# Kernel optimization log

Hardware: AMD Instinct MI355X
Metric: run time of the kernel (lower is better)

## Reference

```python
import jax, jax.numpy as jnp
import numpy as np

Ts = 1.0  # simulation time step from netParams['simulation']


def _alpha_filter(x, tau):
    # Causal SRM-alpha PSP filter along time (leading axis):
    #   y[t] = Ts * sum_{k>=0} (k*Ts/tau) * exp(1 - k*Ts/tau) * x[t-k]
    # Implemented as an exact 2-state linear recurrence (IIR form of the alpha kernel).
    d = jnp.float32(np.exp(-Ts / tau))
    c = jnp.float32(np.e * Ts / tau * Ts)  # kernel scale * Ts integration factor

    def step(carry, xt):
        P, Q = carry           # P[t] = sum x[j] d^{t-j}; Q[t] = sum x[j] (t-j) d^{t-j}
        Q = d * (Q + P)
        P = d * P + xt
        return (P, Q), c * Q

    z = jnp.zeros_like(x[0])
    _, y = jax.lax.scan(step, (z, z), x)
    return y


def _make_spike(theta, tauRho, scaleRho):
    # SLAYER spike function: Heaviside forward, surrogate-gradient backward
    pdf_scale = scaleRho / (tauRho * theta)
    pdf_tc = tauRho * theta

    @jax.custom_vjp
    def spike(u):
        return (u >= theta).astype(u.dtype)

    def fwd(u):
        return spike(u), u

    def bwd(u, g):
        return (g * pdf_scale * jnp.exp(-jnp.abs(u - theta) / pdf_tc),)

    spike.defvjp(fwd, bwd)
    return spike


def _lif_spike(u_in, theta, tauRef, scaleRef, tauRho, scaleRho):
    # Sequential leaky integrate-and-fire with alpha refractory kernel:
    #   u[t] = u_in[t] - scaleRef*theta * sum_{j<t} s[j] * (dt/tauRef)*exp(1-dt/tauRef), dt=(t-j)*Ts
    # Refractory alpha kernel realized by the same 2-state recurrence, fed by emitted spikes.
    d = jnp.float32(np.exp(-Ts / tauRef))
    ref_gain = jnp.float32(scaleRef * theta * np.e * Ts / tauRef)
    spike = _make_spike(theta, tauRho, scaleRho)

    def step(carry, ut):
        P, Q = carry
        Q = d * (Q + P)            # refractory kernel value (zero at lag 0)
        s = spike(ut - ref_gain * Q)
        P = d * P + s              # inject this step's spikes
        return (P, Q), s

    z = jnp.zeros_like(u_in[0])
    _, s = jax.lax.scan(step, (z, z), u_in)
    return s


def _conv2d_t(x, w, pad):
    # x: [T, N, C, H, W] -> same spatial conv applied at every timestep (slayer conv = Conv3d with kT=1)
    T, N, C, H, W = x.shape
    y = jax.lax.conv_general_dilated(
        x.reshape(T * N, C, H, W), w,
        window_strides=(1, 1), padding=[(pad, pad), (pad, pad)],
        dimension_numbers=('NCHW', 'OIHW', 'NCHW'))
    return y.reshape(T, N, -1, H, W)


def _forward(spikeInput, conv1_w, conv2_w):
    # spikeInput: [N, C, H, W, T] -> scan over leading time axis
    x = jnp.transpose(spikeInput, (4, 0, 1, 2, 3))
    psp1 = _alpha_filter(x, tau=1.0)                                        # slayer1.psp (tauSr=1)
    s1 = _lif_spike(_conv2d_t(psp1, conv1_w, 2),
                    theta=30.0, tauRef=1.0, scaleRef=1.0, tauRho=1.0, scaleRho=10.0)
    psp2 = _alpha_filter(s1, tau=2.0)                                       # slayer2.psp (tauSr=2)
    s2 = _lif_spike(_conv2d_t(psp2, conv2_w, 1),
                    theta=50.0, tauRef=2.0, scaleRef=1.0, tauRho=1.0, scaleRho=10.0)
    return jnp.transpose(s2, (1, 2, 3, 4, 0))  # back to [N, C, H, W, T]


def setup_inputs() -> dict:
    key = jax.random.key(0)
    k1, k2, k3 = jax.random.split(key, 3)
    spikeInput = (jax.random.uniform(k1, (2, 8, 128, 128, 64)) < 0.1).astype(jnp.float32)
    # slayer conv uses weightScale-amplified weights, bias-free; scale so thresholds are reachable
    conv1_w = jax.random.normal(k2, (8, 8, 5, 5), jnp.float32) * 2.0
    conv2_w = jax.random.normal(k3, (8, 8, 3, 3), jnp.float32) * 2.0
    return {"spikeInput": spikeInput, "conv1_w": conv1_w, "conv2_w": conv2_w}


def reference(spikeInput, conv1_w, conv2_w):
    return _forward(spikeInput, conv1_w, conv2_w)
```

## Files before the change

kernel.cpp:

```cpp
#include <hip/hip_runtime.h>

#define TN 64
#define NB 2
#define CH 8
#define HH 128
#define WW 128
#define HW (HH*WW)
#define CHW (CH*HW)
#define NCHW (NB*CHW)


__global__ __launch_bounds__(256) void k_tr(const float* __restrict__ x,
                                            unsigned char* __restrict__ xT) {
    __shared__ unsigned char lds[256 * 68];
    const int tid = threadIdx.x;
    const size_t e0 = (size_t)blockIdx.x * 256;
    const float4* xb = reinterpret_cast<const float4*>(x + (e0 + tid) * TN);
    unsigned int* lds32 = reinterpret_cast<unsigned int*>(lds);
    #pragma unroll
    for (int k = 0; k < 16; ++k) {
        float4 v = xb[k];
        unsigned int p = ((unsigned)v.x) | (((unsigned)v.y) << 8) |
                         (((unsigned)v.z) << 16) | (((unsigned)v.w) << 24);
        lds32[tid * 17 + k] = p;
    }
    __syncthreads();
    const int lane = tid & 63, w = tid >> 6;
    #pragma unroll
    for (int k = 0; k < 16; ++k) {
        int t = w * 16 + k;
        unsigned int b0 = lds[(4 * lane + 0) * 68 + t];
        unsigned int b1 = lds[(4 * lane + 1) * 68 + t];
        unsigned int b2 = lds[(4 * lane + 2) * 68 + t];
        unsigned int b3 = lds[(4 * lane + 3) * 68 + t];
        unsigned int p = b0 | (b1 << 8) | (b2 << 16) | (b3 << 24);
        *reinterpret_cast<unsigned int*>(xT + (size_t)t * NCHW + e0 + 4 * lane) = p;
    }
}

__global__ __launch_bounds__(256, 4) void k_conv1(const unsigned char* __restrict__ in,
                                                  const float* __restrict__ w1,
                                                  float* __restrict__ outp) {
    __shared__ __align__(16) float tile[2][12][136];
    const int img = blockIdx.y;
    const int h0 = blockIdx.x * 8;
    const int tid = threadIdx.x;
    const int yi = tid >> 5;
    const int x0 = (tid & 31) * 4;
    const unsigned char* base = in + (size_t)img * CHW;

    int goff[7];
    #pragma unroll
    for (int k = 0; k < 7; ++k) {
        int idx = tid + (k << 8);
        int r = idx / 136;
        int c = idx - r * 136;
        int gh = h0 + r - 2, gw = c - 2;
        bool ok = (idx < 1632) && (gh >= 0) && (gh < HH) && (gw >= 0) && (gw < WW);
        goff[k] = ok ? (gh * WW + gw) : -1;
    }

    float va[7];
    #pragma unroll
    for (int k = 0; k < 7; ++k) {
        int g = goff[k];
        int gc = g < 0 ? 0 : g;
        float t0 = (float)base[gc];
        va[k] = g < 0 ? 0.f : t0;
    }

    float acc[CH][4];
    #pragma unroll
    for (int co = 0; co < CH; ++co)
        #pragma unroll
        for (int xo = 0; xo < 4; ++xo) acc[co][xo] = 0.f;

    for (int ci = 0; ci < CH; ++ci) {
        float* dst = &tile[ci & 1][0][0];
        #pragma unroll
        for (int k = 0; k < 7; ++k) {
            int idx = tid + (k << 8);
            if (k < 6 || idx < 1632) dst[idx] = va[k];
        }
        if (ci < 7) {
            const unsigned char* nb = base + (size_t)(ci + 1) * HW;
            #pragma unroll
            for (int k = 0; k < 7; ++k) {
                int g = goff[k];
                int gc = g < 0 ? 0 : g;
                float t0 = (float)nb[gc];
                va[k] = g < 0 ? 0.f : t0;
            }
        }
        __syncthreads();

        const float* chp = &tile[ci & 1][0][0];
        #pragma unroll
        for (int ky = 0; ky < 5; ++ky) {
            const float4* rp =
                reinterpret_cast<const float4*>(chp + (yi + ky) * 136 + x0);
            float4 A = rp[0], B = rp[1];
            float f[8] = {A.x, A.y, A.z, A.w, B.x, B.y, B.z, B.w};
            #pragma unroll
            for (int co = 0; co < CH; ++co) {
                const float* wp = w1 + (co * CH + ci) * 25 + ky * 5;
                #pragma unroll
                for (int kx = 0; kx < 5; ++kx) {
                    float wv = wp[kx];
                    #pragma unroll
                    for (int xo = 0; xo < 4; ++xo)
                        acc[co][xo] = fmaf(wv, f[kx + xo], acc[co][xo]);
                }
            }
        }
    }

    float* ob = outp + (size_t)img * CHW + (h0 + yi) * WW + x0;
    #pragma unroll
    for (int co = 0; co < CH; ++co)
        *reinterpret_cast<float4*>(ob + co * HW) =
            make_float4(acc[co][0], acc[co][1], acc[co][2], acc[co][3]);
}

__global__ __launch_bounds__(256) void k_alif1(const float* __restrict__ v1,
                                               unsigned char* __restrict__ s1) {
    int e2 = blockIdx.x * blockDim.x + threadIdx.x;
    if (e2 >= NCHW / 2) return;
    const float d1 = 0.36787944117144233f;
    const float c1 = 2.7182818284590452f;
    const float dr = 0.36787944117144233f;
    const float rg = 81.54845485377136f;
    const float th = 30.f;
    float P0 = 0.f, Q0 = 0.f, Pr0 = 0.f, Qr0 = 0.f;
    float P1 = 0.f, Q1 = 0.f, Pr1 = 0.f, Qr1 = 0.f;
    const float2* ve = reinterpret_cast<const float2*>(v1);
    #pragma unroll 8
    for (int t = 0; t < TN; ++t) {
        float2 v = ve[(size_t)t * (NCHW / 2) + e2];
        Q0 = d1 * (Q0 + P0); P0 = d1 * P0 + v.x;
        Qr0 = dr * (Qr0 + Pr0);
        float s0 = (c1 * Q0 - rg * Qr0 >= th) ? 1.0f : 0.0f;
        Pr0 = dr * Pr0 + s0;
        Q1 = d1 * (Q1 + P1); P1 = d1 * P1 + v.y;
        Qr1 = dr * (Qr1 + Pr1);
        float s1v = (c1 * Q1 - rg * Qr1 >= th) ? 1.0f : 0.0f;
        Pr1 = dr * Pr1 + s1v;
        uchar2 o; o.x = (unsigned char)s0; o.y = (unsigned char)s1v;
        *reinterpret_cast<uchar2*>(s1 + (size_t)t * NCHW + 2 * e2) = o;
    }
}

__global__ __launch_bounds__(256, 4) void k_conv2(const unsigned char* __restrict__ in,
                                                  const float* __restrict__ w2,
                                                  float* __restrict__ outp) {
    __shared__ __align__(16) float tile[2][10][136];
    const int img = blockIdx.y;
    const int h0 = blockIdx.x * 8;
    const int tid = threadIdx.x;
    const int yi = tid >> 5;
    const int x0 = (tid & 31) * 4;
    const unsigned char* base = in + (size_t)img * CHW;

    int goff[6];
    #pragma unroll
    for (int k = 0; k < 6; ++k) {
        int idx = tid + (k << 8);
        int r = idx / 136;
        int c = idx - r * 136;
        int gh = h0 + r - 1, gw = c - 1;
        bool ok = (idx < 1360) && (gh >= 0) && (gh < HH) && (gw >= 0) && (gw < WW);
        goff[k] = ok ? (gh * WW + gw) : -1;
    }

    float va[6];
    #pragma unroll
    for (int k = 0; k < 6; ++k) {
        int g = goff[k];
        int gc = g < 0 ? 0 : g;
        float t0 = (float)base[gc];
        va[k] = g < 0 ? 0.f : t0;
    }

    float acc[CH][4];
    #pragma unroll
    for (int co = 0; co < CH; ++co)
        #pragma unroll
        for (int xo = 0; xo < 4; ++xo) acc[co][xo] = 0.f;

    for (int ci = 0; ci < CH; ++ci) {
        float* dst = &tile[ci & 1][0][0];
        #pragma unroll
        for (int k = 0; k < 6; ++k) {
            int idx = tid + (k << 8);
            if (k < 5 || idx < 1360) dst[idx] = va[k];
        }
        if (ci < 7) {
            const unsigned char* nb = base + (size_t)(ci + 1) * HW;
            #pragma unroll
            for (int k = 0; k < 6; ++k) {
                int g = goff[k];
                int gc = g < 0 ? 0 : g;
                float t0 = (float)nb[gc];
                va[k] = g < 0 ? 0.f : t0;
            }
        }
        __syncthreads();

        const float* chp = &tile[ci & 1][0][0];
        #pragma unroll
        for (int ky = 0; ky < 3; ++ky) {
            const float4* rp =
                reinterpret_cast<const float4*>(chp + (yi + ky) * 136 + x0);
            float4 A = rp[0], B = rp[1];
            float f[8] = {A.x, A.y, A.z, A.w, B.x, B.y, B.z, B.w};
            #pragma unroll
            for (int co = 0; co < CH; ++co) {
                const float* wp = w2 + (co * CH + ci) * 9 + ky * 3;
                #pragma unroll
                for (int kx = 0; kx < 3; ++kx) {
                    float wv = wp[kx];
                    #pragma unroll
                    for (int xo = 0; xo < 4; ++xo)
                        acc[co][xo] = fmaf(wv, f[kx + xo], acc[co][xo]);
                }
            }
        }
    }

    float* ob = outp + (size_t)img * CHW + (h0 + yi) * WW + x0;
    #pragma unroll
    for (int co = 0; co < CH; ++co)
        *reinterpret_cast<float4*>(ob + co * HW) =
            make_float4(acc[co][0], acc[co][1], acc[co][2], acc[co][3]);
}

__global__ __launch_bounds__(256) void k_alif2(const float* __restrict__ v2,
                                               float* __restrict__ outp) {
    int e = blockIdx.x * blockDim.x + threadIdx.x;
    if (e >= NCHW) return;
    const float d2 = 0.60653065971263342f;
    const float c2 = 1.35914091422952262f;
    const float dr = 0.60653065971263342f;
    const float rg = 67.95704571147613f;
    const float th = 50.f;
    float P = 0.f, Q = 0.f, Pr = 0.f, Qr = 0.f;
    float sv[TN];
    #pragma unroll
    for (int t = 0; t < TN; ++t) {
        Q = d2 * (Q + P);
        P = d2 * P + v2[(size_t)t * NCHW + e];
        Qr = dr * (Qr + Pr);
        float s = (c2 * Q - rg * Qr >= th) ? 1.0f : 0.0f;
        Pr = dr * Pr + s;
        sv[t] = s;
    }
    float4* o = reinterpret_cast<float4*>(outp + (size_t)e * TN);
    #pragma unroll
    for (int i = 0; i < TN / 4; ++i)
        o[i] = make_float4(sv[4 * i], sv[4 * i + 1], sv[4 * i + 2], sv[4 * i + 3]);
}

extern "C" void kernel_launch(void* const* d_in, const int* in_sizes, int n_in,
                              void* d_out, int out_size, void* d_ws, size_t ws_size,
                              hipStream_t stream) {
    const float* x  = (const float*)d_in[0];
    const float* w1 = (const float*)d_in[1];
    const float* w2 = (const float*)d_in[2];
    float* out = (float*)d_out;

    float* vbuf = (float*)d_ws;
    unsigned char* xT = (unsigned char*)d_ws + (size_t)TN * NCHW * 4;
    unsigned char* s1 = xT + (size_t)TN * NCHW;

    dim3 blk(256);
    dim3 grd_pt(NCHW / 256);
    dim3 grd_pt2(NCHW / 512);
    dim3 grd_cv(16, TN * NB);

    k_tr<<<grd_pt, blk, 0, stream>>>(x, xT);
    k_conv1<<<grd_cv, blk, 0, stream>>>(xT, w1, vbuf);
    k_alif1<<<grd_pt2, blk, 0, stream>>>(vbuf, s1);
    k_conv2<<<grd_cv, blk, 0, stream>>>(s1, w2, vbuf);
    k_alif2<<<grd_pt, blk, 0, stream>>>(vbuf, out);
}
```

Before: 180.8 us.

## Stage all input channels as bytes in shared memory with a single barrier

Both convolution kernels now load all eight input channels of the halo tile into shared memory as uint8 values up front, followed by one barrier. This replaces the double-buffered float tile that synchronised once per channel. Each thread reads two 32-bit words per row and unpacks the bytes to floats in registers, which cuts shared-memory footprint and removes seven of the eight barriers. The cost is byte-extraction and int-to-float conversion work in the inner loop, and all global loads are issued before any compute starts instead of overlapping with it.

```diff
diff --git a/kernel.cpp b/kernel.cpp
--- a/kernel.cpp
+++ b/kernel.cpp
@@ -41,7 +41,7 @@
 __global__ __launch_bounds__(256, 4) void k_conv1(const unsigned char* __restrict__ in,
                                                   const float* __restrict__ w1,
                                                   float* __restrict__ outp) {
-    __shared__ __align__(16) float tile[2][12][136];
+    __shared__ __align__(16) unsigned char lds8[CH * 12 * 136];
     const int img = blockIdx.y;
     const int h0 = blockIdx.x * 8;
     const int tid = threadIdx.x;
@@ -60,47 +60,39 @@
         goff[k] = ok ? (gh * WW + gw) : -1;
     }
 
-    float va[7];
-    #pragma unroll
-    for (int k = 0; k < 7; ++k) {
-        int g = goff[k];
-        int gc = g < 0 ? 0 : g;
-        float t0 = (float)base[gc];
-        va[k] = g < 0 ? 0.f : t0;
-    }
-
-    float acc[CH][4];
-    #pragma unroll
-    for (int co = 0; co < CH; ++co)
-        #pragma unroll
-        for (int xo = 0; xo < 4; ++xo) acc[co][xo] = 0.f;
-
-    for (int ci = 0; ci < CH; ++ci) {
-        float* dst = &tile[ci & 1][0][0];
+    #pragma unroll
+    for (int ci = 0; ci < CH; ++ci) {
+        const unsigned char* cb = base + ci * HW;
         #pragma unroll
         for (int k = 0; k < 7; ++k) {
             int idx = tid + (k << 8);
-            if (k < 6 || idx < 1632) dst[idx] = va[k];
-        }
-        if (ci < 7) {
-            const unsigned char* nb = base + (size_t)(ci + 1) * HW;
-            #pragma unroll
-            for (int k = 0; k < 7; ++k) {
+            if (k < 6 || idx < 1632) {
                 int g = goff[k];
                 int gc = g < 0 ? 0 : g;
-                float t0 = (float)nb[gc];
-                va[k] = g < 0 ? 0.f : t0;
-            }
-        }
-        __syncthreads();
-
-        const float* chp = &tile[ci & 1][0][0];
+                unsigned char v = cb[gc];
+                lds8[ci * 1632 + idx] = (g < 0) ? (unsigned char)0 : v;
+            }
+        }
+    }
+    __syncthreads();
+
+    float acc[CH][4];
+    #pragma unroll
+    for (int co = 0; co < CH; ++co)
+        #pragma unroll
+        for (int xo = 0; xo < 4; ++xo) acc[co][xo] = 0.f;
+
+    for (int ci = 0; ci < CH; ++ci) {
+        const unsigned char* cp = lds8 + ci * 1632;
         #pragma unroll
         for (int ky = 0; ky < 5; ++ky) {
-            const float4* rp =
-                reinterpret_cast<const float4*>(chp + (yi + ky) * 136 + x0);
-            float4 A = rp[0], B = rp[1];
-            float f[8] = {A.x, A.y, A.z, A.w, B.x, B.y, B.z, B.w};
+            const unsigned int* p =
+                reinterpret_cast<const unsigned int*>(cp + (yi + ky) * 136 + x0);
+            unsigned int a = p[0], b = p[1];
+            float f[8] = {(float)(a & 0xff), (float)((a >> 8) & 0xff),
+                          (float)((a >> 16) & 0xff), (float)(a >> 24),
+                          (float)(b & 0xff), (float)((b >> 8) & 0xff),
+                          (float)((b >> 16) & 0xff), (float)(b >> 24)};
             #pragma unroll
             for (int co = 0; co < CH; ++co) {
                 const float* wp = w1 + (co * CH + ci) * 25 + ky * 5;
@@ -153,7 +145,7 @@
 __global__ __launch_bounds__(256, 4) void k_conv2(const unsigned char* __restrict__ in,
                                                   const float* __restrict__ w2,
                                                   float* __restrict__ outp) {
-    __shared__ __align__(16) float tile[2][10][136];
+    __shared__ __align__(16) unsigned char lds8[CH * 10 * 136];
     const int img = blockIdx.y;
     const int h0 = blockIdx.x * 8;
     const int tid = threadIdx.x;
@@ -172,47 +164,39 @@
         goff[k] = ok ? (gh * WW + gw) : -1;
     }
 
-    float va[6];
-    #pragma unroll
-    for (int k = 0; k < 6; ++k) {
-        int g = goff[k];
-        int gc = g < 0 ? 0 : g;
-        float t0 = (float)base[gc];
-        va[k] = g < 0 ? 0.f : t0;
-    }
-
-    float acc[CH][4];
-    #pragma unroll
-    for (int co = 0; co < CH; ++co)
-        #pragma unroll
-        for (int xo = 0; xo < 4; ++xo) acc[co][xo] = 0.f;
-
-    for (int ci = 0; ci < CH; ++ci) {
-        float* dst = &tile[ci & 1][0][0];
+    #pragma unroll
+    for (int ci = 0; ci < CH; ++ci) {
+        const unsigned char* cb = base + ci * HW;
         #pragma unroll
         for (int k = 0; k < 6; ++k) {
             int idx = tid + (k << 8);
-            if (k < 5 || idx < 1360) dst[idx] = va[k];
-        }
-        if (ci < 7) {
-            const unsigned char* nb = base + (size_t)(ci + 1) * HW;
-            #pragma unroll
-            for (int k = 0; k < 6; ++k) {
+            if (k < 5 || idx < 1360) {
                 int g = goff[k];
                 int gc = g < 0 ? 0 : g;
-                float t0 = (float)nb[gc];
-                va[k] = g < 0 ? 0.f : t0;
-            }
-        }
-        __syncthreads();
-
-        const float* chp = &tile[ci & 1][0][0];
+                unsigned char v = cb[gc];
+                lds8[ci * 1360 + idx] = (g < 0) ? (unsigned char)0 : v;
+            }
+        }
+    }
+    __syncthreads();
+
+    float acc[CH][4];
+    #pragma unroll
+    for (int co = 0; co < CH; ++co)
+        #pragma unroll
+        for (int xo = 0; xo < 4; ++xo) acc[co][xo] = 0.f;
+
+    for (int ci = 0; ci < CH; ++ci) {
+        const unsigned char* cp = lds8 + ci * 1360;
         #pragma unroll
         for (int ky = 0; ky < 3; ++ky) {
-            const float4* rp =
-                reinterpret_cast<const float4*>(chp + (yi + ky) * 136 + x0);
-            float4 A = rp[0], B = rp[1];
-            float f[8] = {A.x, A.y, A.z, A.w, B.x, B.y, B.z, B.w};
+            const unsigned int* p =
+                reinterpret_cast<const unsigned int*>(cp + (yi + ky) * 136 + x0);
+            unsigned int a = p[0], b = p[1];
+            float f[8] = {(float)(a & 0xff), (float)((a >> 8) & 0xff),
+                          (float)((a >> 16) & 0xff), (float)(a >> 24),
+                          (float)(b & 0xff), (float)((b >> 8) & 0xff),
+                          (float)((b >> 16) & 0xff), (float)(b >> 24)};
             #pragma unroll
             for (int co = 0; co < CH; ++co) {
                 const float* wp = w2 + (co * CH + ci) * 9 + ky * 3;
```

Result: no change. 178.9 us (median of 2 runs) (-1.1%).
